# Optimization experiments

Hardware: AMD Instinct MI355X
Metric: run time of the kernel (lower is better)

The kernel has to match this reference:

```python
import jax, jax.numpy as jnp
import numpy as np

T, B, D, H = 1024, 64, 256, 256  # seq_len, batch, input_dim, hidden_dim (== n_qubits)


def setup_inputs() -> dict:
    key = jax.random.key(0)
    k_x, k_w, k_b, k_n = jax.random.split(key, 4)
    inputs = jax.random.normal(k_x, (T, B, D), dtype=jnp.float32)
    # Four gate Linears (forget, input, update, output) fused into one [D+H, 4H] matrix.
    # Math is identical to 4 separate Linears on the same `combined` input.
    bound = 1.0 / np.sqrt(D + H)
    W = jax.random.uniform(k_w, (D + H, 4 * H), dtype=jnp.float32, minval=-bound, maxval=bound)
    b = jax.random.uniform(k_b, (4 * H,), dtype=jnp.float32, minval=-bound, maxval=bound)
    beta = jnp.float32(0.01)  # learnable noise_beta parameter
    noise = jax.random.normal(k_n, (T, B, H), dtype=jnp.float32)  # randn_like(hx) per step
    return {"inputs": inputs, "W": W, "b": b, "beta": beta, "noise": noise}


def reference(inputs, W, b, beta, noise):
    Bsz = inputs.shape[1]
    Hd = W.shape[1] // 4
    h0 = jnp.zeros((Bsz, Hd), dtype=inputs.dtype)
    c0 = jnp.zeros((Bsz, Hd), dtype=inputs.dtype)

    def step(carry, xs):
        hx, cx = carry
        x, nz = xs
        combined = jnp.concatenate([x, hx], axis=1)          # [B, D+H]
        gates = combined @ W + b                             # [B, 4H] fused gate GEMM
        f, i, g, o = jnp.split(gates, 4, axis=1)
        f = jax.nn.sigmoid(f)
        i = jax.nn.sigmoid(i)
        g = jnp.tanh(g)
        o = jax.nn.sigmoid(o)
        cx_new = f * cx + i * g
        hx_new = o * jnp.tanh(cx_new) + beta * nz            # noise injection
        return (hx_new, cx_new), hx_new

    (hx, cx), outputs = jax.lax.scan(step, (h0, c0), (inputs, noise))
    return outputs, hx, cx
```

## Files before the change

### kernel.cpp

```cpp
#include <hip/hip_runtime.h>


typedef _Float16 half2_t __attribute__((ext_vector_type(2)));
typedef _Float16 half4_t __attribute__((ext_vector_type(4)));
typedef _Float16 half8_t __attribute__((ext_vector_type(8)));
typedef float floatx4 __attribute__((ext_vector_type(4)));

__device__ __forceinline__ float fdot2(unsigned h, unsigned w, float acc) {
#if __has_builtin(__builtin_amdgcn_fdot2)
  return __builtin_amdgcn_fdot2(__builtin_bit_cast(half2_t, h),
                                __builtin_bit_cast(half2_t, w), acc, false);
#else
  half2_t a = __builtin_bit_cast(half2_t, h);
  half2_t b = __builtin_bit_cast(half2_t, w);
  return acc + (float)a[0] * (float)b[0] + (float)a[1] * (float)b[1];
#endif
}

__device__ __forceinline__ floatx4 mfma16x16x32(half8_t a, half8_t b, floatx4 c) {
#if __has_builtin(__builtin_amdgcn_mfma_f32_16x16x32_f16)
  return __builtin_amdgcn_mfma_f32_16x16x32_f16(a, b, c, 0, 0, 0);
#else
  half4_t alo = __builtin_shufflevector(a, a, 0, 1, 2, 3);
  half4_t ahi = __builtin_shufflevector(a, a, 4, 5, 6, 7);
  half4_t blo = __builtin_shufflevector(b, b, 0, 1, 2, 3);
  half4_t bhi = __builtin_shufflevector(b, b, 4, 5, 6, 7);
  c = __builtin_amdgcn_mfma_f32_16x16x16f16(alo, blo, c, 0, 0, 0);
  c = __builtin_amdgcn_mfma_f32_16x16x16f16(ahi, bhi, c, 0, 0, 0);
  return c;
#endif
}

__device__ __forceinline__ float sigm(float x) { return 1.f / (1.f + __expf(-x)); }
__device__ __forceinline__ float tanh_(float x) {
  float ax = fabsf(x);
  float e = __expf(-2.f * ax);
  float t = (1.f - e) / (1.f + e);
  return x < 0.f ? -t : t;
}

__global__ __launch_bounds__(256) void k_transpose_w(const float* __restrict__ W,
                                                     _Float16* __restrict__ WT) {
  __shared__ float tile[64][65];
  const int bx = blockIdx.x & 15;
  const int by = blockIdx.x >> 4;
  const int c0 = bx * 64, r0 = by * 64;
  const int tid = threadIdx.x;
#pragma unroll
  for (int i = 0; i < 16; ++i) {
    int idx = tid + i * 256;
    int r = idx >> 6, c = idx & 63;
    tile[r][c] = W[(size_t)(r0 + r) * 1024 + c0 + c];
  }
  __syncthreads();
#pragma unroll
  for (int i = 0; i < 16; ++i) {
    int idx = tid + i * 256;
    int c = idx >> 6, r = idx & 63;
    WT[(size_t)(c0 + c) * 512 + r0 + r] = (_Float16)tile[r][c];
  }
}

__global__ __launch_bounds__(256) void k_gx_gemm(const float* __restrict__ X,
                                                 const _Float16* __restrict__ WT,
                                                 const float* __restrict__ bias,
                                                 _Float16* __restrict__ Gx) {
  const int nb = blockIdx.x & 7;
  const int mb = blockIdx.x >> 3;
  const int m0 = mb * 128, n0 = nb * 128;
  __shared__ __align__(16) _Float16 As[128 * 40];
  __shared__ __align__(16) _Float16 Bs[128 * 40];
  const int tid = threadIdx.x;
  const int wave = tid >> 6, lane = tid & 63;
  const int wm = (wave >> 1) * 64, wn = (wave & 1) * 64;
  const int lm = lane & 15, lg = lane >> 4;
  const int srow = tid >> 1, skh = (tid & 1) * 16;
  floatx4 acc[4][4] = {};
  for (int kt = 0; kt < 256; kt += 32) {
    __syncthreads();
    {
      const float* src = X + (size_t)(m0 + srow) * 256 + kt + skh;
      float4 f0 = ((const float4*)src)[0];
      float4 f1 = ((const float4*)src)[1];
      float4 f2 = ((const float4*)src)[2];
      float4 f3 = ((const float4*)src)[3];
      half8_t h0 = {(_Float16)f0.x, (_Float16)f0.y, (_Float16)f0.z, (_Float16)f0.w,
                    (_Float16)f1.x, (_Float16)f1.y, (_Float16)f1.z, (_Float16)f1.w};
      half8_t h1 = {(_Float16)f2.x, (_Float16)f2.y, (_Float16)f2.z, (_Float16)f2.w,
                    (_Float16)f3.x, (_Float16)f3.y, (_Float16)f3.z, (_Float16)f3.w};
      *(half8_t*)&As[srow * 40 + skh] = h0;
      *(half8_t*)&As[srow * 40 + skh + 8] = h1;
      const _Float16* bsrc = WT + (size_t)(n0 + srow) * 512 + kt + skh;
      half8_t b0 = ((const half8_t*)bsrc)[0];
      half8_t b1 = ((const half8_t*)bsrc)[1];
      *(half8_t*)&Bs[srow * 40 + skh] = b0;
      *(half8_t*)&Bs[srow * 40 + skh + 8] = b1;
    }
    __syncthreads();
    half8_t af[4], bf[4];
#pragma unroll
    for (int mf = 0; mf < 4; ++mf)
      af[mf] = *(const half8_t*)&As[(wm + mf * 16 + lm) * 40 + lg * 8];
#pragma unroll
    for (int nf = 0; nf < 4; ++nf)
      bf[nf] = *(const half8_t*)&Bs[(wn + nf * 16 + lm) * 40 + lg * 8];
#pragma unroll
    for (int mf = 0; mf < 4; ++mf)
#pragma unroll
      for (int nf = 0; nf < 4; ++nf)
        acc[mf][nf] = mfma16x16x32(af[mf], bf[nf], acc[mf][nf]);
  }
#pragma unroll
  for (int mf = 0; mf < 4; ++mf) {
#pragma unroll
    for (int nf = 0; nf < 4; ++nf) {
      const int gm = m0 + wm + mf * 16 + lg * 4;
      const int gn = n0 + wn + nf * 16 + lm;
      const float bv = bias[gn];
#pragma unroll
      for (int i = 0; i < 4; ++i)
        Gx[(size_t)(gm + i) * 1024 + gn] = (_Float16)(acc[mf][nf][i] + bv);
    }
  }
}

__global__ __attribute__((amdgpu_flat_work_group_size(512, 512),
                          amdgpu_waves_per_eu(2, 2))) void
k_lstm(const _Float16* __restrict__ Gx, const _Float16* __restrict__ WT,
       const float* __restrict__ noise, const float* __restrict__ beta_p,
       float* __restrict__ out) {
  __shared__ __align__(16) uint4 wl[1024 * 9];
  __shared__ float gates[1024];
  __shared__ unsigned hx2[128];

  const int b = blockIdx.x;
  const int tid = threadIdx.x;
  const float beta = beta_p[0];
  const int c0 = tid, c1 = tid + 512;

  const uint4* p0 = (const uint4*)(WT + (size_t)c0 * 512 + 256);
  const uint4* p1 = (const uint4*)(WT + (size_t)c1 * 512 + 256);
  uint4 w0[23], w1[23];
#pragma unroll
  for (int i = 0; i < 23; ++i) w0[i] = p0[i];
#pragma unroll
  for (int i = 0; i < 23; ++i) w1[i] = p1[i];
  uint4* wlp0 = wl + c0 * 9;
  uint4* wlp1 = wl + c1 * 9;
#pragma unroll
  for (int i = 0; i < 9; ++i) wlp0[i] = p0[23 + i];
#pragma unroll
  for (int i = 0; i < 9; ++i) wlp1[i] = p1[23 + i];
  if (tid < 128) hx2[tid] = 0u;
  float cx = 0.f, hlast = 0.f;
  __syncthreads();

  const _Float16* gp0 = Gx + (size_t)b * 1024 + c0;
  const _Float16* gp1 = Gx + (size_t)b * 1024 + c1;
  const float* nzp = noise + (size_t)b * 256 + (tid & 255);
  float* outp = out + (size_t)b * 256 + tid;

  float g0 = (float)gp0[0];
  float g1 = (float)gp1[0];
  float nz = nzp[0];

  for (int t = 0; t < 1024; ++t) {
    float g0n = 0.f, g1n = 0.f, nzn = 0.f;
    if (t < 1023) {
      g0n = (float)gp0[65536];
      g1n = (float)gp1[65536];
      nzn = nzp[16384];
    }

    float a0e = 0.f, a0o = 0.f, a1e = 0.f, a1o = 0.f;
#pragma unroll
    for (int i = 0; i < 23; ++i) {
      uint4 h4 = *(const uint4*)&hx2[i * 4];
      a0e = fdot2(h4.x, w0[i].x, a0e);
      a0o = fdot2(h4.y, w0[i].y, a0o);
      a0e = fdot2(h4.z, w0[i].z, a0e);
      a0o = fdot2(h4.w, w0[i].w, a0o);
      a1e = fdot2(h4.x, w1[i].x, a1e);
      a1o = fdot2(h4.y, w1[i].y, a1o);
      a1e = fdot2(h4.z, w1[i].z, a1e);
      a1o = fdot2(h4.w, w1[i].w, a1o);
    }
#pragma unroll
    for (int i = 0; i < 9; ++i) {
      uint4 h4 = *(const uint4*)&hx2[92 + i * 4];
      uint4 wa = wlp0[i];
      uint4 wb = wlp1[i];
      a0e = fdot2(h4.x, wa.x, a0e);
      a0o = fdot2(h4.y, wa.y, a0o);
      a0e = fdot2(h4.z, wa.z, a0e);
      a0o = fdot2(h4.w, wa.w, a0o);
      a1e = fdot2(h4.x, wb.x, a1e);
      a1o = fdot2(h4.y, wb.y, a1o);
      a1e = fdot2(h4.z, wb.z, a1e);
      a1o = fdot2(h4.w, wb.w, a1o);
    }
    gates[c0] = a0e + a0o + g0;
    gates[c1] = a1e + a1o + g1;
    __syncthreads();

    if (tid < 256) {
      float f = sigm(gates[tid]);
      float ii = sigm(gates[tid + 256]);
      float gg = tanh_(gates[tid + 512]);
      float oo = sigm(gates[tid + 768]);
      cx = f * cx + ii * gg;
      float h = oo * tanh_(cx) + beta * nz;
      hlast = h;
      outp[0] = h;
      ((_Float16*)hx2)[tid] = (_Float16)h;
    }
    g0 = g0n; g1 = g1n; nz = nzn;
    gp0 += 65536; gp1 += 65536; nzp += 16384; outp += 16384;
    __syncthreads();
  }

  if (tid < 256) {
    out[(size_t)16777216 + (size_t)b * 256 + tid] = hlast;
    out[(size_t)16777216 + 16384 + (size_t)b * 256 + tid] = cx;
  }
}

extern "C" void kernel_launch(void* const* d_in, const int* in_sizes, int n_in,
                              void* d_out, int out_size, void* d_ws, size_t ws_size,
                              hipStream_t stream) {
  const float* X = (const float*)d_in[0];
  const float* W = (const float*)d_in[1];
  const float* bias = (const float*)d_in[2];
  const float* beta = (const float*)d_in[3];
  const float* noise = (const float*)d_in[4];
  float* out = (float*)d_out;

  char* ws = (char*)d_ws;
  _Float16* Gx = (_Float16*)ws;
  _Float16* WT = (_Float16*)(ws + (size_t)134217728);

  k_transpose_w<<<128, 256, 0, stream>>>(W, WT);
  k_gx_gemm<<<4096, 256, 0, stream>>>(X, WT, bias, Gx);
  k_lstm<<<64, 512, 0, stream>>>(Gx, WT, noise, beta, out);
}
```

Baseline: 1.782 ms.

## Use 1024 threads per LSTM block with one gate column per thread

The recurrent kernel now launches 1024 threads per batch row instead of 512, and each thread computes one gate column instead of two. Per-thread register weights are halved (23 uint4 instead of 46), which shortens each thread's serial dot-product chain per timestep and allows more waves per SIMD. The cost is more threads taking part in each block-wide barrier, and the waves_per_eu hint is dropped, so register allocation is left to the compiler.

```diff
diff --git a/kernel.cpp b/kernel.cpp
--- a/kernel.cpp
+++ b/kernel.cpp
@@ -124,8 +124,7 @@
   }
 }
 
-__global__ __attribute__((amdgpu_flat_work_group_size(512, 512),
-                          amdgpu_waves_per_eu(2, 2))) void
+__global__ __attribute__((amdgpu_flat_work_group_size(1024, 1024))) void
 k_lstm(const _Float16* __restrict__ Gx, const _Float16* __restrict__ WT,
        const float* __restrict__ noise, const float* __restrict__ beta_p,
        float* __restrict__ out) {
@@ -136,71 +135,51 @@
   const int b = blockIdx.x;
   const int tid = threadIdx.x;
   const float beta = beta_p[0];
-  const int c0 = tid, c1 = tid + 512;
-
-  const uint4* p0 = (const uint4*)(WT + (size_t)c0 * 512 + 256);
-  const uint4* p1 = (const uint4*)(WT + (size_t)c1 * 512 + 256);
-  uint4 w0[23], w1[23];
-#pragma unroll
-  for (int i = 0; i < 23; ++i) w0[i] = p0[i];
-#pragma unroll
-  for (int i = 0; i < 23; ++i) w1[i] = p1[i];
-  uint4* wlp0 = wl + c0 * 9;
-  uint4* wlp1 = wl + c1 * 9;
-#pragma unroll
-  for (int i = 0; i < 9; ++i) wlp0[i] = p0[23 + i];
-#pragma unroll
-  for (int i = 0; i < 9; ++i) wlp1[i] = p1[23 + i];
+
+  const uint4* p = (const uint4*)(WT + (size_t)tid * 512 + 256);
+  uint4 w[23];
+#pragma unroll
+  for (int i = 0; i < 23; ++i) w[i] = p[i];
+  uint4* wlp = wl + tid * 9;
+#pragma unroll
+  for (int i = 0; i < 9; ++i) wlp[i] = p[23 + i];
   if (tid < 128) hx2[tid] = 0u;
   float cx = 0.f, hlast = 0.f;
   __syncthreads();
 
-  const _Float16* gp0 = Gx + (size_t)b * 1024 + c0;
-  const _Float16* gp1 = Gx + (size_t)b * 1024 + c1;
+  const _Float16* gp = Gx + (size_t)b * 1024 + tid;
   const float* nzp = noise + (size_t)b * 256 + (tid & 255);
-  float* outp = out + (size_t)b * 256 + tid;
-
-  float g0 = (float)gp0[0];
-  float g1 = (float)gp1[0];
-  float nz = nzp[0];
+  float* outp = out + (size_t)b * 256 + (tid & 255);
+
+  float g = (float)gp[0];
+  float nz = (tid < 256) ? nzp[0] : 0.f;
 
   for (int t = 0; t < 1024; ++t) {
-    float g0n = 0.f, g1n = 0.f, nzn = 0.f;
+    float gn = 0.f, nzn = 0.f;
     if (t < 1023) {
-      g0n = (float)gp0[65536];
-      g1n = (float)gp1[65536];
-      nzn = nzp[16384];
-    }
-
-    float a0e = 0.f, a0o = 0.f, a1e = 0.f, a1o = 0.f;
+      gn = (float)gp[65536];
+      if (tid < 256) nzn = nzp[16384];
+    }
+
+    float ae = 0.f, ao = 0.f;
 #pragma unroll
     for (int i = 0; i < 23; ++i) {
       uint4 h4 = *(const uint4*)&hx2[i * 4];
-      a0e = fdot2(h4.x, w0[i].x, a0e);
-      a0o = fdot2(h4.y, w0[i].y, a0o);
-      a0e = fdot2(h4.z, w0[i].z, a0e);
-      a0o = fdot2(h4.w, w0[i].w, a0o);
-      a1e = fdot2(h4.x, w1[i].x, a1e);
-      a1o = fdot2(h4.y, w1[i].y, a1o);
-      a1e = fdot2(h4.z, w1[i].z, a1e);
-      a1o = fdot2(h4.w, w1[i].w, a1o);
+      ae = fdot2(h4.x, w[i].x, ae);
+      ao = fdot2(h4.y, w[i].y, ao);
+      ae = fdot2(h4.z, w[i].z, ae);
+      ao = fdot2(h4.w, w[i].w, ao);
     }
 #pragma unroll
     for (int i = 0; i < 9; ++i) {
       uint4 h4 = *(const uint4*)&hx2[92 + i * 4];
-      uint4 wa = wlp0[i];
-      uint4 wb = wlp1[i];
-      a0e = fdot2(h4.x, wa.x, a0e);
-      a0o = fdot2(h4.y, wa.y, a0o);
-      a0e = fdot2(h4.z, wa.z, a0e);
-      a0o = fdot2(h4.w, wa.w, a0o);
-      a1e = fdot2(h4.x, wb.x, a1e);
-      a1o = fdot2(h4.y, wb.y, a1o);
-      a1e = fdot2(h4.z, wb.z, a1e);
-      a1o = fdot2(h4.w, wb.w, a1o);
-    }
-    gates[c0] = a0e + a0o + g0;
-    gates[c1] = a1e + a1o + g1;
+      uint4 wa = wlp[i];
+      ae = fdot2(h4.x, wa.x, ae);
+      ao = fdot2(h4.y, wa.y, ao);
+      ae = fdot2(h4.z, wa.z, ae);
+      ao = fdot2(h4.w, wa.w, ao);
+    }
+    gates[tid] = ae + ao + g;
     __syncthreads();
 
     if (tid < 256) {
@@ -214,8 +193,11 @@
       outp[0] = h;
       ((_Float16*)hx2)[tid] = (_Float16)h;
     }
-    g0 = g0n; g1 = g1n; nz = nzn;
-    gp0 += 65536; gp1 += 65536; nzp += 16384; outp += 16384;
+    g = gn;
+    nz = nzn;
+    gp += 65536;
+    nzp += 16384;
+    outp += 16384;
     __syncthreads();
   }
 
@@ -241,5 +223,5 @@
 
   k_transpose_w<<<128, 256, 0, stream>>>(W, WT);
   k_gx_gemm<<<4096, 256, 0, stream>>>(X, WT, bias, Gx);
-  k_lstm<<<64, 512, 0, stream>>>(Gx, WT, noise, beta, out);
-}
+  k_lstm<<<64, 1024, 0, stream>>>(Gx, WT, noise, beta, out);
+}
```

Measured after the change: 2.136 ms. 19.9% more time.
